# Performance work log

Measured on AMD Instinct MI355X. Metric: run time of the kernel, lower is better.

## Reference

```python
import jax, jax.numpy as jnp
import numpy as np

NUM_CLASSES = 4
SIGMA_S = 1.0
SIGMA_Z = 1.0


def _rbf_gram(x, sigma):
    # x: [N, d] -> [N, N] Gaussian kernel exp(-||xi-xj||^2 / (2 sigma^2))
    sq = jnp.sum(x * x, axis=-1)
    d2 = sq[:, None] + sq[None, :] - 2.0 * (x @ x.T)
    d2 = jnp.maximum(d2, 0.0)
    return jnp.exp(-d2 / (2.0 * sigma * sigma))


def _double_center(K):
    # Faithful to: K = mean_center(K, dim=0); K_m = mean_center(K.t(), dim=0)
    K = K - jnp.mean(K, axis=0, keepdims=True)
    K = K.T
    K = K - jnp.mean(K, axis=0, keepdims=True)
    return K


def setup_inputs() -> dict:
    key = jax.random.key(0)
    kz, ks = jax.random.split(key)
    z = jax.random.normal(kz, (8192, 128), dtype=jnp.float32)
    s = jax.random.randint(ks, (8192,), 0, NUM_CLASSES, dtype=jnp.int64)
    norm = jnp.float32(1.0)
    return {"z": z, "s": s, "norm": norm}


def reference(z, s, norm):
    n = z.shape[0]
    s_onehot = jax.nn.one_hot(s, NUM_CLASSES, dtype=z.dtype)  # format_onehot
    K_sm = _double_center(_rbf_gram(s_onehot, SIGMA_S))
    K_zm = _double_center(_rbf_gram(z, SIGMA_Z))
    # trace(K_zm.T @ K_sm) == sum(K_zm * K_sm): O(N^2) instead of O(N^3)
    dep = jnp.sum(K_zm * K_sm)
    dep = dep / (norm * (n * n))
    return dep
```

## Files before the change

kernel.cpp:

```cpp
#include <hip/hip_runtime.h>
#include <hip/hip_bf16.h>

typedef short bf16x8 __attribute__((ext_vector_type(8)));
typedef float f32x4  __attribute__((ext_vector_type(4)));

#define ZD      128
#define BT      128
#define D2_CUT  60.0f
#define D2_TRIG 62.0f

__device__ __forceinline__ unsigned short f2bf(float x) {
    unsigned u = __float_as_uint(x);
    u = (u + 0x7FFFu + ((u >> 16) & 1u)) >> 16;
    return (unsigned short)u;
}

__global__ __launch_bounds__(256) void dep_prep(
    const float* __restrict__ z, const int* __restrict__ s,
    float* __restrict__ sq, float* __restrict__ sqmin,
    unsigned short* __restrict__ zb, float* __restrict__ pvals,
    const float* __restrict__ norm, float* __restrict__ out, int N)
{
    __shared__ float part[64][33];
    const int tid  = threadIdx.x;
    const int wave = tid >> 6, lane = tid & 63;
    const int half = lane >> 5, c = lane & 31;
    const int r0   = blockIdx.x * 64;

    if (blockIdx.x == 0 && wave == 2) {
        int c0 = 0, c1 = 0, c2 = 0, c3 = 0;
        for (int it = lane; it < N / 4; it += 64) {
            int4 v = ((const int4*)s)[it];
            c0 += (v.x == 0) + (v.y == 0) + (v.z == 0) + (v.w == 0);
            c1 += (v.x == 1) + (v.y == 1) + (v.z == 1) + (v.w == 1);
            c2 += (v.x == 2) + (v.y == 2) + (v.z == 2) + (v.w == 2);
            c3 += (v.x == 3) + (v.y == 3) + (v.z == 3) + (v.w == 3);
        }
        #pragma unroll
        for (int off = 1; off < 64; off <<= 1) {
            c0 += __shfl_xor(c0, off, 64);
            c1 += __shfl_xor(c1, off, 64);
            c2 += __shfl_xor(c2, off, 64);
            c3 += __shfl_xor(c3, off, 64);
        }
        if (lane == 0) {
            const double n = (double)N;
            const double p0 = c0 / n, p1 = c1 / n, p2 = c2 / n, p3 = c3 / n;
            const double sump2 = p0*p0 + p1*p1 + p2*p2 + p3*p3;
            const double scale = (1.0 - exp(-1.0)) / ((double)norm[0] * n * n);
            pvals[0] = (float)p0; pvals[1] = (float)p1;
            pvals[2] = (float)p2; pvals[3] = (float)p3;
            pvals[4] = (float)sump2;
            pvals[5] = (float)scale;
            const double c2sum = (double)c0*c0 + (double)c1*c1
                               + (double)c2*c2 + (double)c3*c3;
            const double diag = n - c2sum / n;
            out[0] = (float)(diag * scale);
        }
    }

    #pragma unroll
    for (int i = 0; i < 8; ++i) {
        const int rloc = wave * 16 + i * 2 + half;
        const int r    = r0 + rloc;
        float4 v = ((const float4*)z)[r * 32 + c];
        ushort4 u;
        u.x = f2bf(v.x); u.y = f2bf(v.y); u.z = f2bf(v.z); u.w = f2bf(v.w);
        ((ushort4*)zb)[r * 32 + c] = u;
        part[rloc][c] = v.x*v.x + v.y*v.y + v.z*v.z + v.w*v.w;
    }
    __syncthreads();

    if (wave == 0) {
        float sum = 0.f;
        #pragma unroll
        for (int k = 0; k < 32; ++k) sum += part[lane][k];
        sq[r0 + lane] = sum;
        float mn = sum;
        #pragma unroll
        for (int off = 1; off < 64; off <<= 1)
            mn = fminf(mn, __shfl_xor(mn, off, 64));
        if (lane == 0) sqmin[blockIdx.x] = mn;
    }
}

__global__ __launch_bounds__(256, 2) void dep_pair(
    const unsigned short* __restrict__ zb, const float* __restrict__ sq,
    const float* __restrict__ sqmin, const int* __restrict__ s,
    const float* __restrict__ pvals, float* __restrict__ out, int T)
{
    __shared__ unsigned short Apan[BT * ZD];
    __shared__ unsigned short Bpan[BT * ZD];

    const int tid = threadIdx.x;

    const int t = blockIdx.x;
    #define TRI_BASE(x) ((x) * T - ((x) * ((x) - 1)) / 2)
    double disc = (2.0 * T + 1.0) * (2.0 * T + 1.0) - 8.0 * (double)t;
    int ti = (int)((2.0 * T + 1.0 - sqrt(disc)) * 0.5);
    if (ti < 0) ti = 0;
    if (ti > T - 1) ti = T - 1;
    while (ti + 1 < T && TRI_BASE(ti + 1) <= t) ++ti;
    while (ti > 0 && TRI_BASE(ti) > t) --ti;
    const int tj = ti + (t - TRI_BASE(ti));
    #undef TRI_BASE

    const int i0 = ti * BT, j0 = tj * BT;

    #pragma unroll
    for (int i = 0; i < 8; ++i) {
        const int L   = i * 256 + tid;
        const int row = L >> 4, ch = L & 15;
        const int dst = row * ZD + (((ch ^ (row & 15)) << 3));
        uint4 a = ((const uint4*)(zb + (size_t)i0 * ZD))[L];
        uint4 b = ((const uint4*)(zb + (size_t)j0 * ZD))[L];
        *(uint4*)(Apan + dst) = a;
        *(uint4*)(Bpan + dst) = b;
    }
    __syncthreads();

    const int wave = tid >> 6, lane = tid & 63;
    const int wi = wave >> 1, wj = wave & 1;
    const int l15 = lane & 15, quad = lane >> 4;

    f32x4 accv[4][4];
    #pragma unroll
    for (int a = 0; a < 4; ++a)
        #pragma unroll
        for (int b = 0; b < 4; ++b)
            accv[a][b] = (f32x4){0.f, 0.f, 0.f, 0.f};

    #pragma unroll
    for (int kc = 0; kc < 4; ++kc) {
        bf16x8 af[4], bfr[4];
        const int ch = (quad + 4 * kc) ^ l15;
        #pragma unroll
        for (int it = 0; it < 4; ++it) {
            const int row = wi * 64 + it * 16 + l15;
            af[it] = *(const bf16x8*)(Apan + row * ZD + (ch << 3));
        }
        #pragma unroll
        for (int jt = 0; jt < 4; ++jt) {
            const int row = wj * 64 + jt * 16 + l15;
            bfr[jt] = *(const bf16x8*)(Bpan + row * ZD + (ch << 3));
        }
        #pragma unroll
        for (int it = 0; it < 4; ++it)
            #pragma unroll
            for (int jt = 0; jt < 4; ++jt)
                accv[it][jt] = __builtin_amdgcn_mfma_f32_16x16x32_bf16(
                    af[it], bfr[jt], accv[it][jt], 0, 0, 0);
    }

    float m = -1e30f;
    #pragma unroll
    for (int it = 0; it < 4; ++it)
        #pragma unroll
        for (int jt = 0; jt < 4; ++jt) {
            const f32x4 v = accv[it][jt];
            m = fmaxf(m, fmaxf(fmaxf(v[0], v[1]), fmaxf(v[2], v[3])));
        }
    #pragma unroll
    for (int off = 1; off < 64; off <<= 1)
        m = fmaxf(m, __shfl_xor(m, off, 64));

    const float bound = sqmin[ti * 2 + wi] + sqmin[tj * 2 + wj] - 2.0f * m;

    if (bound < D2_TRIG) {
        const float p0 = pvals[0], p1 = pvals[1],
                    p2 = pvals[2], p3 = pvals[3];
        const float sump2 = pvals[4], scale = pvals[5];
        const float p[4] = {p0, p1, p2, p3};

        const int ibase = i0 + wi * 64, jbase = j0 + wj * 64;
        float sqj[4];
        #pragma unroll
        for (int jt = 0; jt < 4; ++jt) sqj[jt] = sq[jbase + jt * 16 + l15];

        float local = 0.f;
        #pragma unroll
        for (int it = 0; it < 4; ++it) {
            #pragma unroll
            for (int r = 0; r < 4; ++r) {
                const int i = ibase + it * 16 + quad * 4 + r;
                const float sqi = sq[i];
                #pragma unroll
                for (int jt = 0; jt < 4; ++jt) {
                    const int j = jbase + jt * 16 + l15;
                    float d2 = sqi + sqj[jt] - 2.0f * accv[it][jt][r];
                    d2 = fmaxf(d2, 0.0f);
                    if (d2 < D2_CUT && i != j) {
                        const int si = s[i], sj = s[j];
                        const float w = (si == sj ? 1.0f : 0.0f)
                                      - p[si] - p[sj] + sump2;
                        local += w * __expf(-0.5f * d2);
                    }
                }
            }
        }
        if (ti < tj) local *= 2.0f;

        #pragma unroll
        for (int off = 32; off > 0; off >>= 1)
            local += __shfl_down(local, off, 64);
        if (lane == 0 && local != 0.0f)
            atomicAdd(out, local * scale);
    }
}

extern "C" void kernel_launch(void* const* d_in, const int* in_sizes, int n_in,
                              void* d_out, int out_size, void* d_ws, size_t ws_size,
                              hipStream_t stream)
{
    const float* z    = (const float*)d_in[0];
    const int*   s    = (const int*)d_in[1];
    const float* norm = (const float*)d_in[2];
    float* out = (float*)d_out;

    const int N = in_sizes[1];
    const int T = N / BT;
    const int nPrep = N / 64;

    char* ws = (char*)d_ws;
    float*          pvals = (float*)ws;
    float*          sq    = (float*)(ws + 64);
    float*          sqmin = (float*)(ws + 64 + (size_t)N * 4);
    unsigned short* zb    = (unsigned short*)(ws + 64 + (size_t)N * 4
                                              + (size_t)nPrep * 4 + 48);

    dep_prep<<<nPrep, 256, 0, stream>>>(z, s, sq, sqmin, zb, pvals,
                                        norm, out, N);
    const int nblocks = T * (T + 1) / 2;
    dep_pair<<<nblocks, 256, 0, stream>>>(zb, sq, sqmin, s, pvals, out, T);
}
```

Before: 84.80 us.

## Load pair-kernel panels with direct global-to-LDS async copies; halve prep block size

The tile-pair kernel now fills its A/B LDS panels with global_load_lds 16-byte copies instead of staging through registers. The XOR swizzle moves from the LDS write address to the global read address. The prep kernel processes 32 rows per block, which doubles the grid, and stores row-norm minima per 32 rows; the pair kernel combines two of them for each 64-row wave bound. This is meant to cut register traffic and load latency in the panel fill and to spread prep work over more CUs. It depends on the compiler waiting on the async loads before the barrier.

```diff
diff --git a/kernel.cpp b/kernel.cpp
--- a/kernel.cpp
+++ b/kernel.cpp
@@ -13,6 +13,14 @@
     unsigned u = __float_as_uint(x);
     u = (u + 0x7FFFu + ((u >> 16) & 1u)) >> 16;
     return (unsigned short)u;
+}
+
+__device__ __forceinline__ void async_copy16(const unsigned short* g,
+                                             unsigned short* l) {
+    __builtin_amdgcn_global_load_lds(
+        (const __attribute__((address_space(1))) unsigned int*)g,
+        (__attribute__((address_space(3))) unsigned int*)l,
+        16, 0, 0);
 }
 
 __global__ __launch_bounds__(256) void dep_prep(
@@ -21,11 +29,11 @@
     unsigned short* __restrict__ zb, float* __restrict__ pvals,
     const float* __restrict__ norm, float* __restrict__ out, int N)
 {
-    __shared__ float part[64][33];
+    __shared__ float part[32][33];
     const int tid  = threadIdx.x;
     const int wave = tid >> 6, lane = tid & 63;
     const int half = lane >> 5, c = lane & 31;
-    const int r0   = blockIdx.x * 64;
+    const int r0   = blockIdx.x * 32;
 
     if (blockIdx.x == 0 && wave == 2) {
         int c0 = 0, c1 = 0, c2 = 0, c3 = 0;
@@ -60,8 +68,8 @@
     }
 
     #pragma unroll
-    for (int i = 0; i < 8; ++i) {
-        const int rloc = wave * 16 + i * 2 + half;
+    for (int i = 0; i < 4; ++i) {
+        const int rloc = wave * 8 + i * 2 + half;
         const int r    = r0 + rloc;
         float4 v = ((const float4*)z)[r * 32 + c];
         ushort4 u;
@@ -71,14 +79,14 @@
     }
     __syncthreads();
 
-    if (wave == 0) {
+    if (wave == 0 && lane < 32) {
         float sum = 0.f;
         #pragma unroll
         for (int k = 0; k < 32; ++k) sum += part[lane][k];
         sq[r0 + lane] = sum;
         float mn = sum;
         #pragma unroll
-        for (int off = 1; off < 64; off <<= 1)
+        for (int off = 1; off < 32; off <<= 1)
             mn = fminf(mn, __shfl_xor(mn, off, 64));
         if (lane == 0) sqmin[blockIdx.x] = mn;
     }
@@ -92,7 +100,8 @@
     __shared__ unsigned short Apan[BT * ZD];
     __shared__ unsigned short Bpan[BT * ZD];
 
-    const int tid = threadIdx.x;
+    const int tid  = threadIdx.x;
+    const int wave = tid >> 6, lane = tid & 63;
 
     const int t = blockIdx.x;
     #define TRI_BASE(x) ((x) * T - ((x) * ((x) - 1)) / 2)
@@ -107,19 +116,23 @@
 
     const int i0 = ti * BT, j0 = tj * BT;
 
-    #pragma unroll
-    for (int i = 0; i < 8; ++i) {
-        const int L   = i * 256 + tid;
-        const int row = L >> 4, ch = L & 15;
-        const int dst = row * ZD + (((ch ^ (row & 15)) << 3));
-        uint4 a = ((const uint4*)(zb + (size_t)i0 * ZD))[L];
-        uint4 b = ((const uint4*)(zb + (size_t)j0 * ZD))[L];
-        *(uint4*)(Apan + dst) = a;
-        *(uint4*)(Bpan + dst) = b;
+    {
+        const unsigned short* gAp = zb + (size_t)i0 * ZD;
+        const unsigned short* gBp = zb + (size_t)j0 * ZD;
+        const int rl  = lane >> 4;
+        const int c   = lane & 15;
+        #pragma unroll
+        for (int k = 0; k < 8; ++k) {
+            const int r0i = (wave * 8 + k) * 4;
+            const int row = r0i + rl;
+            const int gch = c ^ (row & 15);
+            const size_t go = (size_t)row * ZD + (gch << 3);
+            async_copy16(gAp + go, Apan + r0i * ZD);
+            async_copy16(gBp + go, Bpan + r0i * ZD);
+        }
     }
     __syncthreads();
 
-    const int wave = tid >> 6, lane = tid & 63;
     const int wi = wave >> 1, wj = wave & 1;
     const int l15 = lane & 15, quad = lane >> 4;
 
@@ -164,7 +177,11 @@
     for (int off = 1; off < 64; off <<= 1)
         m = fmaxf(m, __shfl_xor(m, off, 64));
 
-    const float bound = sqmin[ti * 2 + wi] + sqmin[tj * 2 + wj] - 2.0f * m;
+    const int gA = (i0 >> 5) + wi * 2;
+    const int gB = (j0 >> 5) + wj * 2;
+    const float sminA = fminf(sqmin[gA], sqmin[gA + 1]);
+    const float sminB = fminf(sqmin[gB], sqmin[gB + 1]);
+    const float bound = sminA + sminB - 2.0f * m;
 
     if (bound < D2_TRIG) {
         const float p0 = pvals[0], p1 = pvals[1],
@@ -219,17 +236,16 @@
 
     const int N = in_sizes[1];
     const int T = N / BT;
-    const int nPrep = N / 64;
 
     char* ws = (char*)d_ws;
     float*          pvals = (float*)ws;
     float*          sq    = (float*)(ws + 64);
     float*          sqmin = (float*)(ws + 64 + (size_t)N * 4);
     unsigned short* zb    = (unsigned short*)(ws + 64 + (size_t)N * 4
-                                              + (size_t)nPrep * 4 + 48);
-
-    dep_prep<<<nPrep, 256, 0, stream>>>(z, s, sq, sqmin, zb, pvals,
-                                        norm, out, N);
+                                              + (size_t)(N / 32) * 4);
+
+    dep_prep<<<N / 32, 256, 0, stream>>>(z, s, sq, sqmin, zb, pvals,
+                                         norm, out, N);
     const int nblocks = T * (T + 1) / 2;
     dep_pair<<<nblocks, 256, 0, stream>>>(zb, sq, sqmin, s, pvals, out, T);
 }
```

Measured after the change: 82.30 us. 2.9% less time.
